# Optimization experiments

Measured on AMD Instinct MI355X. Metric: run time of the kernel, lower is better.

The kernel has to match this reference:

```python
import jax, jax.numpy as jnp
import numpy as np

D_MODEL = 1024
NUM_HEADS = 16
HEAD_DIM = D_MODEL // NUM_HEADS
SEQ_LEN = 2048
THETA = 10000.0


def setup_inputs() -> dict:
    key = jax.random.key(0)
    ks = jax.random.split(key, 9)
    s = 1.0 / np.sqrt(D_MODEL)
    inp = {
        "x": jax.random.normal(ks[0], (2, SEQ_LEN, D_MODEL), dtype=jnp.float32),
        "Wq": jax.random.uniform(ks[1], (D_MODEL, D_MODEL), jnp.float32, -s, s),
        "bq": jax.random.uniform(ks[2], (D_MODEL,), jnp.float32, -s, s),
        "Wk": jax.random.uniform(ks[3], (D_MODEL, D_MODEL), jnp.float32, -s, s),
        "bk": jax.random.uniform(ks[4], (D_MODEL,), jnp.float32, -s, s),
        "Wv": jax.random.uniform(ks[5], (D_MODEL, D_MODEL), jnp.float32, -s, s),
        "bv": jax.random.uniform(ks[6], (D_MODEL,), jnp.float32, -s, s),
        "Wo": jax.random.uniform(ks[7], (D_MODEL, D_MODEL), jnp.float32, -s, s),
        "bo": jax.random.uniform(ks[8], (D_MODEL,), jnp.float32, -s, s),
    }
    return inp


def _rope_cos_sin(seq_len, dim, theta):
    inv_freq = 1.0 / theta ** (jnp.arange(0, dim, 2, dtype=jnp.float32) / dim)  # [dim/2]
    t = jnp.arange(seq_len, dtype=jnp.float32)
    freqs = jnp.outer(t, inv_freq)  # [S, dim/2]
    return jnp.cos(freqs), jnp.sin(freqs)


def _apply_rope(x, cos, sin):
    # x: [B, H, S, head_dim]; interleaved complex pairs (even, odd)
    x2 = x.reshape(*x.shape[:-1], -1, 2)  # [B,H,S,hd/2,2]
    xe, xo = x2[..., 0], x2[..., 1]
    c = cos[None, None, :, :]
    s = sin[None, None, :, :]
    oe = xe * c - xo * s
    oo = xe * s + xo * c
    return jnp.stack([oe, oo], axis=-1).reshape(x.shape)


def reference(x, Wq, bq, Wk, bk, Wv, bv, Wo, bo):
    B, S, D = x.shape
    H, hd = NUM_HEADS, HEAD_DIM
    q = x @ Wq.T + bq
    k = x @ Wk.T + bk
    v = x @ Wv.T + bv
    # [B, H, S, hd]
    q = q.reshape(B, S, H, hd).transpose(0, 2, 1, 3)
    k = k.reshape(B, S, H, hd).transpose(0, 2, 1, 3)
    v = v.reshape(B, S, H, hd).transpose(0, 2, 1, 3)
    cos, sin = _rope_cos_sin(S, hd, THETA)
    q = _apply_rope(q, cos, sin)
    k = _apply_rope(k, cos, sin)
    scores = jnp.einsum("bhqd,bhkd->bhqk", q, k) / jnp.sqrt(jnp.float32(hd))
    causal = jnp.triu(jnp.ones((S, S), dtype=bool), k=1)
    scores = jnp.where(causal[None, None, :, :], -jnp.inf, scores)
    attn = jax.nn.softmax(scores, axis=-1)
    out = jnp.einsum("bhqk,bhkd->bhqd", attn, v)
    out = out.transpose(0, 2, 1, 3).reshape(B, S, D)
    return out @ Wo.T + bo
```

## Files before the change

### kernel.cpp

```cpp
#include <hip/hip_runtime.h>
#include <hip/hip_bf16.h>

#define S_LEN 2048
#define DM 1024
#define NH 16
#define HD 64
#define M_ROWS 4096
#define LOG2E 1.4426950408889634f
#define MASKVAL -1.0e4f
#define QSCALE 0.18033688011112042f

typedef __attribute__((ext_vector_type(8))) short short8;
typedef __attribute__((ext_vector_type(4))) float f32x4;
typedef __attribute__((ext_vector_type(16))) float f32x16;

__device__ inline ushort f2b(float f) {
  union { float f; unsigned u; } v; v.f = f;
  unsigned r = v.u + 0x7fffu + ((v.u >> 16) & 1u);
  return (ushort)(r >> 16);
}

__device__ inline float b2f(ushort u) {
  union { unsigned u; float f; } v; v.u = ((unsigned)u) << 16; return v.f;
}

__device__ inline unsigned pk_bf16(float a, float b) {
  __hip_bfloat162 h = __float22bfloat162_rn(make_float2(a, b));
  union { __hip_bfloat162 h; unsigned u; } v; v.h = h;
  return v.u;
}

__device__ inline float fexp2(float x) { return __builtin_amdgcn_exp2f(x); }

__device__ inline void gl_lds16(const void* g, void* l) {
  __builtin_amdgcn_global_load_lds(
      (const __attribute__((address_space(1))) void*)g,
      (__attribute__((address_space(3))) void*)l, 16, 0, 0);
}

__global__ __launch_bounds__(256) void cast_rope_kernel(
    const float* __restrict__ x, const float* __restrict__ Wq, const float* __restrict__ Wk,
    const float* __restrict__ Wv, const float* __restrict__ Wo,
    ushort* __restrict__ xb, ushort* __restrict__ Wqb, ushort* __restrict__ Wkb,
    ushort* __restrict__ Wvb, ushort* __restrict__ Wob,
    float* __restrict__ ropeC, float* __restrict__ ropeS) {
  const int bid = blockIdx.x;
  if (bid >= 8192) {
    int idx = (bid - 8192) * 256 + threadIdx.x;
    int s = idx >> 5, i = idx & 31;
    float inv = exp2f(-(float)i * (13.287712379549449f / 32.0f));
    float a = (float)s * inv;
    ropeC[idx] = cosf(a);
    ropeS[idx] = sinf(a);
    return;
  }
  int i = bid * 256 + threadIdx.x;
  int r = i >> 18, off = i & 0x3FFFF;
  const float4* s;
  uint2* d;
  switch (r) {
    case 0: case 1: case 2: case 3: s = (const float4*)x + i;  d = (uint2*)xb + i;  break;
    case 4: s = (const float4*)Wq + off; d = (uint2*)Wqb + off; break;
    case 5: s = (const float4*)Wk + off; d = (uint2*)Wkb + off; break;
    case 6: s = (const float4*)Wv + off; d = (uint2*)Wvb + off; break;
    default: s = (const float4*)Wo + off; d = (uint2*)Wob + off; break;
  }
  float4 v = *s;
  uint2 o;
  o.x = pk_bf16(v.x, v.y);
  o.y = pk_bf16(v.z, v.w);
  *d = o;
}

__global__ __launch_bounds__(256) void gemm_qkv_kernel(const ushort* __restrict__ xb,
    const ushort* __restrict__ Wqb, const ushort* __restrict__ Wkb, const ushort* __restrict__ Wvb,
    const float* __restrict__ bq, const float* __restrict__ bk, const float* __restrict__ bv,
    const float* __restrict__ ropeC, const float* __restrict__ ropeS,
    ushort* __restrict__ qb, ushort* __restrict__ kb, ushort* __restrict__ vT) {
  __shared__ ushort lds[128 * 136];
  ushort* As = lds;
  ushort* Bs = lds + 8192;
  const int z = blockIdx.z;
  const ushort* W = (z == 0) ? Wqb : ((z == 1) ? Wkb : Wvb);
  const float* bias = (z == 0) ? bq : ((z == 1) ? bk : bv);
  const int m0 = blockIdx.x * 128, n0 = blockIdx.y * 128;
  const int t = threadIdx.x, lane = t & 63, wave = t >> 6;
  const int wr = (wave >> 1) * 64, wc = (wave & 1) * 64;
  const int lr = lane & 15, lg = lane >> 4;

  int rows_[4], gs_[4], slots_[4];
#pragma unroll
  for (int j = 0; j < 4; j++) {
    const int slot = wave * 256 + j * 64 + lane;
    slots_[j] = slot;
    rows_[j] = slot >> 3;
    gs_[j] = (slot & 7) ^ (rows_[j] & 7);
  }

  f32x4 acc[4][4];
#pragma unroll
  for (int a = 0; a < 4; a++)
#pragma unroll
    for (int b = 0; b < 4; b++) acc[a][b] = (f32x4){0.f, 0.f, 0.f, 0.f};

  for (int k0 = 0; k0 < DM; k0 += 64) {
    __syncthreads();
#pragma unroll
    for (int j = 0; j < 4; j++)
      gl_lds16(&xb[(size_t)(m0 + rows_[j]) * DM + k0 + gs_[j] * 8], &As[slots_[j] * 8]);
#pragma unroll
    for (int j = 0; j < 4; j++)
      gl_lds16(&W[(size_t)(n0 + rows_[j]) * DM + k0 + gs_[j] * 8], &Bs[slots_[j] * 8]);
    __syncthreads();
#pragma unroll
    for (int s32 = 0; s32 < 2; s32++) {
      short8 af[4], bf[4];
#pragma unroll
      for (int mt = 0; mt < 4; mt++) {
        const int row = wr + mt * 16 + lr;
        af[mt] = *(const short8*)&As[(row * 8 + ((s32 * 4 + lg) ^ (row & 7))) * 8];
      }
#pragma unroll
      for (int nt = 0; nt < 4; nt++) {
        const int row = wc + nt * 16 + lr;
        bf[nt] = *(const short8*)&Bs[(row * 8 + ((s32 * 4 + lg) ^ (row & 7))) * 8];
      }
#pragma unroll
      for (int mt = 0; mt < 4; mt++)
#pragma unroll
        for (int nt = 0; nt < 4; nt++)
          acc[mt][nt] = __builtin_amdgcn_mfma_f32_16x16x32_bf16(af[mt], bf[nt], acc[mt][nt], 0, 0, 0);
    }
  }

  __syncthreads();
#pragma unroll
  for (int mt = 0; mt < 4; mt++) {
#pragma unroll
    for (int nt = 0; nt < 4; nt++) {
      const int nloc = wc + nt * 16 + lr;
      const float bn = bias[n0 + nloc];
#pragma unroll
      for (int r = 0; r < 4; r++) {
        const int mloc = wr + mt * 16 + lg * 4 + r;
        const ushort v = f2b(acc[mt][nt][r] + bn);
        if (z < 2) lds[mloc * 136 + nloc] = v;
        else       lds[nloc * 136 + mloc] = v;
      }
    }
  }
  __syncthreads();

  const int b = m0 >> 11;
  if (z < 2) {
    ushort* dst = (z == 0) ? qb : kb;
    const float qscale = (z == 0) ? QSCALE : 1.0f;
#pragma unroll
    for (int c = 0; c < 8; c++) {
      const int sloc = c * 16 + (t >> 4);
      const int nloc = (t & 15) * 8;
      short8 val = *(const short8*)&lds[sloc * 136 + nloc];
      const int s = (m0 + sloc) & (S_LEN - 1);
      const int h = (n0 + nloc) >> 6;
      const int d0 = nloc & 63;
      const float4 cv = *(const float4*)&ropeC[s * 32 + d0 / 2];
      const float4 sv = *(const float4*)&ropeS[s * 32 + d0 / 2];
      uint4 o;
      {
        float e = b2f((ushort)val[0]), od = b2f((ushort)val[1]);
        o.x = pk_bf16((e * cv.x - od * sv.x) * qscale, (e * sv.x + od * cv.x) * qscale);
      }
      {
        float e = b2f((ushort)val[2]), od = b2f((ushort)val[3]);
        o.y = pk_bf16((e * cv.y - od * sv.y) * qscale, (e * sv.y + od * cv.y) * qscale);
      }
      {
        float e = b2f((ushort)val[4]), od = b2f((ushort)val[5]);
        o.z = pk_bf16((e * cv.z - od * sv.z) * qscale, (e * sv.z + od * cv.z) * qscale);
      }
      {
        float e = b2f((ushort)val[6]), od = b2f((ushort)val[7]);
        o.w = pk_bf16((e * cv.w - od * sv.w) * qscale, (e * sv.w + od * cv.w) * qscale);
      }
      *(uint4*)&dst[(((size_t)b * NH + h) * S_LEN + s) * HD + d0] = o;
    }
  } else {
    const int sbase = m0 & (S_LEN - 1);
#pragma unroll
    for (int c = 0; c < 8; c++) {
      const int nloc = c * 16 + (t >> 4);
      const int s0 = (t & 15) * 8;
      short8 val = *(const short8*)&lds[nloc * 136 + s0];
      const int h = (n0 + nloc) >> 6;
      const int d = nloc & 63;
      *(short8*)&vT[(((size_t)b * NH + h) * HD + d) * S_LEN + sbase + s0] = val;
    }
  }
}

__global__ __launch_bounds__(256) void flash_kernel(const ushort* __restrict__ qb,
                                                    const ushort* __restrict__ kb,
                                                    const ushort* __restrict__ vT,
                                                    ushort* __restrict__ Oh,
                                                    float* __restrict__ lsum) {
  __shared__ ushort Ks[2][4096];
  __shared__ ushort VTs[2][4096];
  const int t = threadIdx.x, lane = t & 63, wave = t >> 6;
  const int q31 = lane & 31, h = lane >> 5;
  const int bh = blockIdx.y;
  const int cid = blockIdx.x;
  const int g = (cid >= 24) ? 3 : (cid >= 12) ? 2 : (cid >= 4) ? 1 : 0;
  const int nc = g + 1;
  const int o = cid - 4 * ((g * (g + 1)) >> 1);
  const int qi = o / nc;
  const int c = o - qi * nc;
  const int qt = g * 4 + qi;
  const int q0 = qt * 128;
  const int ntiles = 2 * qt + 2;
  const int kstart = c * 8;
  const int kend = min(kstart + 8, ntiles);
  const int pidx = bh * 40 + cid;

  const ushort* kbh = kb + (size_t)bh * S_LEN * HD;
  const ushort* vbh = vT + (size_t)bh * HD * S_LEN;

  const int qrow = q0 + wave * 32 + q31;
  const ushort* qptr = qb + ((size_t)bh * S_LEN + qrow) * HD + h * 8;
  short8 qf[4];
#pragma unroll
  for (int s = 0; s < 4; s++) qf[s] = *(const short8*)(qptr + s * 16);

  const int slot0 = wave * 128 + lane, slot1 = slot0 + 64;
  const int row0 = slot0 >> 3, g0 = (slot0 & 7) ^ (row0 & 7);
  const int row1 = slot1 >> 3, g1 = (slot1 & 7) ^ (row1 & 7);
  const int lo0 = wave * 128 * 8, lo1 = lo0 + 64 * 8;

  int foff[4][2];
#pragma unroll
  for (int s = 0; s < 4; s++)
#pragma unroll
    for (int st = 0; st < 2; st++) {
      const int row = st * 32 + q31;
      foff[s][st] = (row * 8 + ((2 * s + h) ^ (row & 7))) * 8;
    }

  {
    const int k00 = kstart * 64;
    gl_lds16(kbh + (size_t)(k00 + row0) * HD + g0 * 8, &Ks[0][lo0]);
    gl_lds16(kbh + (size_t)(k00 + row1) * HD + g1 * 8, &Ks[0][lo1]);
    gl_lds16(vbh + (size_t)row0 * S_LEN + k00 + g0 * 8, &VTs[0][lo0]);
    gl_lds16(vbh + (size_t)row1 * S_LEN + k00 + g1 * 8, &VTs[0][lo1]);
  }
  __syncthreads();

  f32x16 O[2];
#pragma unroll
  for (int st = 0; st < 2; st++)
#pragma unroll
    for (int r = 0; r < 16; r++) O[st][r] = 0.f;
  float lacc = 0.f;
  int cur = 0;

  for (int kt = kstart; kt < kend; kt++) {
    if (kt + 1 < kend) {
      const int k0n = (kt + 1) * 64;
      gl_lds16(kbh + (size_t)(k0n + row0) * HD + g0 * 8, &Ks[cur ^ 1][lo0]);
      gl_lds16(kbh + (size_t)(k0n + row1) * HD + g1 * 8, &Ks[cur ^ 1][lo1]);
      gl_lds16(vbh + (size_t)row0 * S_LEN + k0n + g0 * 8, &VTs[cur ^ 1][lo0]);
      gl_lds16(vbh + (size_t)row1 * S_LEN + k0n + g1 * 8, &VTs[cur ^ 1][lo1]);
    }
    const ushort* Kb = Ks[cur];
    const ushort* Vb = VTs[cur];

    f32x16 sc[2];
#pragma unroll
    for (int st = 0; st < 2; st++)
#pragma unroll
      for (int r = 0; r < 16; r++) sc[st][r] = 0.f;
#pragma unroll
    for (int s = 0; s < 4; s++) {
#pragma unroll
      for (int st = 0; st < 2; st++) {
        const short8 kf = *(const short8*)&Kb[foff[s][st]];
        sc[st] = __builtin_amdgcn_mfma_f32_32x32x16_bf16(kf, qf[s], sc[st], 0, 0, 0);
      }
    }
    if (kt * 64 + 63 > q0 + wave * 32) {
#pragma unroll
      for (int st = 0; st < 2; st++)
#pragma unroll
        for (int r = 0; r < 16; r++) {
          const int kcol = kt * 64 + st * 32 + (r & 3) + 8 * (r >> 2) + 4 * h;
          if (kcol > qrow) sc[st][r] = MASKVAL;
        }
    }
#pragma unroll
    for (int st = 0; st < 2; st++)
#pragma unroll
      for (int r = 0; r < 16; r++) {
        const float p = fexp2(sc[st][r]);
        sc[st][r] = p;
        lacc += p;
      }

    unsigned pp[8][2];
#pragma unroll
    for (int st = 0; st < 2; st++)
#pragma unroll
      for (int rg = 0; rg < 4; rg++) {
        pp[st * 4 + rg][0] = pk_bf16(sc[st][4 * rg + 0], sc[st][4 * rg + 1]);
        pp[st * 4 + rg][1] = pk_bf16(sc[st][4 * rg + 2], sc[st][4 * rg + 3]);
      }
#pragma unroll
    for (int s = 0; s < 4; s++) {
      const unsigned sA0 = pp[2 * s][0], sA1 = pp[2 * s][1];
      const unsigned sB0 = pp[2 * s + 1][0], sB1 = pp[2 * s + 1][1];
      const unsigned send0 = h ? sA0 : sB0;
      const unsigned send1 = h ? sA1 : sB1;
      const unsigned recv0 = (unsigned)__shfl_xor((int)send0, 32);
      const unsigned recv1 = (unsigned)__shfl_xor((int)send1, 32);
      union { unsigned u[4]; short8 v; } pf;
      pf.u[0] = h ? recv0 : sA0;
      pf.u[1] = h ? recv1 : sA1;
      pf.u[2] = h ? sB0 : recv0;
      pf.u[3] = h ? sB1 : recv1;
#pragma unroll
      for (int st = 0; st < 2; st++) {
        const short8 vf = *(const short8*)&Vb[foff[s][st]];
        O[st] = __builtin_amdgcn_mfma_f32_32x32x16_bf16(vf, pf.v, O[st], 0, 0, 0);
      }
    }
    __syncthreads();
    cur ^= 1;
  }

  lacc += __shfl_xor(lacc, 32);

  ushort* obase = Oh + ((size_t)pidx * 128 + wave * 32 + q31) * HD;
#pragma unroll
  for (int st = 0; st < 2; st++)
#pragma unroll
    for (int rg = 0; rg < 4; rg++) {
      const int d0 = st * 32 + 8 * rg + 4 * h;
      uint2 w;
      w.x = pk_bf16(O[st][4 * rg + 0], O[st][4 * rg + 1]);
      w.y = pk_bf16(O[st][4 * rg + 2], O[st][4 * rg + 3]);
      *(uint2*)&obase[d0] = w;
    }
  if (h == 0) lsum[(size_t)pidx * 128 + wave * 32 + q31] = lacc;
}

__global__ __launch_bounds__(256) void combine_kernel(const ushort* __restrict__ Oh,
                                                      const float* __restrict__ lsum,
                                                      ushort* __restrict__ attn) {
  const int tid = blockIdx.x * 256 + threadIdx.x;
  const int d8 = tid & 7;
  const int q = (tid >> 3) & (S_LEN - 1);
  const int bh = tid >> 14;
  const int qt = q >> 7, row = q & 127;
  const int g = qt >> 2, nc = g + 1;
  const int base = 4 * ((g * (g + 1)) >> 1) + (qt & 3) * nc;
  const int p0 = bh * 40 + base;

  float l = 0.f;
  float acc[8];
#pragma unroll
  for (int j = 0; j < 8; j++) acc[j] = 0.f;
  for (int c = 0; c < nc; c++) {
    const size_t rowidx = (size_t)(p0 + c) * 128 + row;
    l += lsum[rowidx];
    const uint4 a = *(const uint4*)&Oh[rowidx * HD + d8 * 8];
    const unsigned au[4] = {a.x, a.y, a.z, a.w};
#pragma unroll
    for (int j = 0; j < 4; j++) {
      acc[2 * j] += b2f((ushort)(au[j] & 0xffff));
      acc[2 * j + 1] += b2f((ushort)(au[j] >> 16));
    }
  }
  const float inv = 1.f / l;
  uint4 o;
  unsigned* op = (unsigned*)&o;
#pragma unroll
  for (int j = 0; j < 4; j++) op[j] = pk_bf16(acc[2 * j] * inv, acc[2 * j + 1] * inv);
  const int b = bh >> 4, hh = bh & 15;
  *(uint4*)&attn[((size_t)b * S_LEN + q) * DM + hh * HD + d8 * 8] = o;
}

__global__ __launch_bounds__(256) void gemm_out_kernel(const ushort* __restrict__ attn,
                                                       const ushort* __restrict__ Wob,
                                                       const float* __restrict__ bo,
                                                       float* __restrict__ out) {
  __shared__ ushort As[4096];
  __shared__ ushort Bs[2048];
  const int m0 = blockIdx.x * 128, n0 = blockIdx.y * 64;
  const int t = threadIdx.x, lane = t & 63, wave = t >> 6;
  const int wm = (wave >> 1) * 64, wn = (wave & 1) * 32;
  const int lr = lane & 15, lg = lane >> 4;
  const int slotA0 = wave * 128 + lane, slotA1 = slotA0 + 64;
  const int rowA0 = slotA0 >> 2, gA0 = (slotA0 & 3) ^ (rowA0 & 3);
  const int rowA1 = slotA1 >> 2, gA1 = (slotA1 & 3) ^ (rowA1 & 3);
  const int slotB = wave * 64 + lane;
  const int rowB = slotB >> 2, gB = (slotB & 3) ^ (rowB & 3);

  f32x4 acc[4][2];
#pragma unroll
  for (int a = 0; a < 4; a++)
#pragma unroll
    for (int b = 0; b < 2; b++) acc[a][b] = (f32x4){0.f, 0.f, 0.f, 0.f};

  for (int k0 = 0; k0 < DM; k0 += 32) {
    __syncthreads();
    gl_lds16(&attn[(size_t)(m0 + rowA0) * DM + k0 + gA0 * 8], &As[slotA0 * 8]);
    gl_lds16(&attn[(size_t)(m0 + rowA1) * DM + k0 + gA1 * 8], &As[slotA1 * 8]);
    gl_lds16(&Wob[(size_t)(n0 + rowB) * DM + k0 + gB * 8], &Bs[slotB * 8]);
    __syncthreads();
    short8 af[4], bf[2];
#pragma unroll
    for (int mt = 0; mt < 4; mt++) {
      const int row = wm + mt * 16 + lr;
      af[mt] = *(const short8*)&As[(row * 4 + (lg ^ (row & 3))) * 8];
    }
#pragma unroll
    for (int nt = 0; nt < 2; nt++) {
      const int row = wn + nt * 16 + lr;
      bf[nt] = *(const short8*)&Bs[(row * 4 + (lg ^ (row & 3))) * 8];
    }
#pragma unroll
    for (int mt = 0; mt < 4; mt++)
#pragma unroll
      for (int nt = 0; nt < 2; nt++)
        acc[mt][nt] = __builtin_amdgcn_mfma_f32_16x16x32_bf16(af[mt], bf[nt], acc[mt][nt], 0, 0, 0);
  }

#pragma unroll
  for (int mt = 0; mt < 4; mt++) {
#pragma unroll
    for (int nt = 0; nt < 2; nt++) {
      const int n = n0 + wn + nt * 16 + lr;
      const float bn = bo[n];
#pragma unroll
      for (int r = 0; r < 4; r++) {
        const int m = m0 + wm + mt * 16 + lg * 4 + r;
        out[(size_t)m * DM + n] = acc[mt][nt][r] + bn;
      }
    }
  }
}

extern "C" void kernel_launch(void* const* d_in, const int* in_sizes, int n_in,
                              void* d_out, int out_size, void* d_ws, size_t ws_size,
                              hipStream_t stream) {
  const float* x  = (const float*)d_in[0];
  const float* Wq = (const float*)d_in[1];
  const float* bq = (const float*)d_in[2];
  const float* Wk = (const float*)d_in[3];
  const float* bk = (const float*)d_in[4];
  const float* Wv = (const float*)d_in[5];
  const float* bv = (const float*)d_in[6];
  const float* Wo = (const float*)d_in[7];
  const float* bo = (const float*)d_in[8];
  float* out = (float*)d_out;

  char* ws = (char*)d_ws;
  size_t off = 0;
  auto alloc = [&](size_t bytes) { char* p = ws + off; off += (bytes + 255) & ~255ull; return p; };
  ushort* xb   = (ushort*)alloc((size_t)M_ROWS * DM * 2);
  ushort* Wqb  = (ushort*)alloc((size_t)DM * DM * 2);
  ushort* Wkb  = (ushort*)alloc((size_t)DM * DM * 2);
  ushort* Wvb  = (ushort*)alloc((size_t)DM * DM * 2);
  ushort* Wob  = (ushort*)alloc((size_t)DM * DM * 2);
  ushort* qb   = (ushort*)alloc((size_t)M_ROWS * DM * 2);
  ushort* kb   = (ushort*)alloc((size_t)M_ROWS * DM * 2);
  ushort* vTb  = (ushort*)alloc((size_t)M_ROWS * DM * 2);
  ushort* attn = (ushort*)alloc((size_t)M_ROWS * DM * 2);
  ushort* Ohb  = (ushort*)alloc((size_t)1280 * 128 * HD * 2);
  float* lsb   = (float*)alloc((size_t)1280 * 128 * 4);
  float* ropeC = (float*)alloc((size_t)S_LEN * 32 * 4);
  float* ropeS = (float*)alloc((size_t)S_LEN * 32 * 4);
  (void)ws_size; (void)in_sizes; (void)n_in; (void)out_size;

  cast_rope_kernel<<<8448, 256, 0, stream>>>(x, Wq, Wk, Wv, Wo, xb, Wqb, Wkb, Wvb, Wob,
                                             ropeC, ropeS);
  gemm_qkv_kernel<<<dim3(M_ROWS / 128, DM / 128, 3), 256, 0, stream>>>(
      xb, Wqb, Wkb, Wvb, bq, bk, bv, ropeC, ropeS, qb, kb, vTb);
  flash_kernel<<<dim3(40, 32), 256, 0, stream>>>(qb, kb, vTb, Ohb, lsb);
  combine_kernel<<<2048, 256, 0, stream>>>(Ohb, lsb, attn);
  gemm_out_kernel<<<dim3(M_ROWS / 128, DM / 64), 256, 0, stream>>>(attn, Wob, bo, out);
}
```

Baseline: 202.3 us.

## Double-buffer LDS tiles in QKV and output projection GEMMs

Both projection GEMMs now prefetch the next K-slice into a second LDS buffer while MFMAs run on the current one, so only one barrier is needed per iteration. The QKV GEMM's K-step drops from 64 to 32 so that two buffers fit within the existing 17408-element LDS array, and the swizzle changes to 4 groups per row. The aim is to overlap global-to-LDS loads with compute. The trade-off is twice as many loop iterations and barriers in the QKV kernel, and it relies on the barrier at the end of each iteration to order the async LDS writes.

```diff
diff --git a/kernel.cpp b/kernel.cpp
--- a/kernel.cpp
+++ b/kernel.cpp
@@ -77,7 +77,7 @@
     const float* __restrict__ bq, const float* __restrict__ bk, const float* __restrict__ bv,
     const float* __restrict__ ropeC, const float* __restrict__ ropeS,
     ushort* __restrict__ qb, ushort* __restrict__ kb, ushort* __restrict__ vT) {
-  __shared__ ushort lds[128 * 136];
+  __shared__ ushort lds[17408];
   ushort* As = lds;
   ushort* Bs = lds + 8192;
   const int z = blockIdx.z;
@@ -88,14 +88,13 @@
   const int wr = (wave >> 1) * 64, wc = (wave & 1) * 64;
   const int lr = lane & 15, lg = lane >> 4;
 
-  int rows_[4], gs_[4], slots_[4];
-#pragma unroll
-  for (int j = 0; j < 4; j++) {
-    const int slot = wave * 256 + j * 64 + lane;
-    slots_[j] = slot;
-    rows_[j] = slot >> 3;
-    gs_[j] = (slot & 7) ^ (rows_[j] & 7);
-  }
+  const int slot0 = wave * 128 + lane, slot1 = slot0 + 64;
+  const int row0 = slot0 >> 2, g0 = (slot0 & 3) ^ (row0 & 3);
+  const int row1 = slot1 >> 2, g1 = (slot1 & 3) ^ (row1 & 3);
+  const ushort* Ap0 = &xb[(size_t)(m0 + row0) * DM + g0 * 8];
+  const ushort* Ap1 = &xb[(size_t)(m0 + row1) * DM + g1 * 8];
+  const ushort* Wp0 = &W[(size_t)(n0 + row0) * DM + g0 * 8];
+  const ushort* Wp1 = &W[(size_t)(n0 + row1) * DM + g1 * 8];
 
   f32x4 acc[4][4];
 #pragma unroll
@@ -103,37 +102,43 @@
 #pragma unroll
     for (int b = 0; b < 4; b++) acc[a][b] = (f32x4){0.f, 0.f, 0.f, 0.f};
 
-  for (int k0 = 0; k0 < DM; k0 += 64) {
+  gl_lds16(Ap0, &As[slot0 * 8]);
+  gl_lds16(Ap1, &As[slot1 * 8]);
+  gl_lds16(Wp0, &Bs[slot0 * 8]);
+  gl_lds16(Wp1, &Bs[slot1 * 8]);
+  __syncthreads();
+
+  int buf = 0;
+  for (int i = 0; i < 32; i++) {
+    if (i + 1 < 32) {
+      const int k0 = (i + 1) * 32;
+      const int bo = (buf ^ 1) * 4096;
+      gl_lds16(Ap0 + k0, &As[bo + slot0 * 8]);
+      gl_lds16(Ap1 + k0, &As[bo + slot1 * 8]);
+      gl_lds16(Wp0 + k0, &Bs[bo + slot0 * 8]);
+      gl_lds16(Wp1 + k0, &Bs[bo + slot1 * 8]);
+    }
+    const int fb = buf * 4096;
+    short8 af[4], bf[4];
+#pragma unroll
+    for (int mt = 0; mt < 4; mt++) {
+      const int row = wr + mt * 16 + lr;
+      af[mt] = *(const short8*)&As[fb + (row * 4 + (lg ^ (row & 3))) * 8];
+    }
+#pragma unroll
+    for (int nt = 0; nt < 4; nt++) {
+      const int row = wc + nt * 16 + lr;
+      bf[nt] = *(const short8*)&Bs[fb + (row * 4 + (lg ^ (row & 3))) * 8];
+    }
+#pragma unroll
+    for (int mt = 0; mt < 4; mt++)
+#pragma unroll
+      for (int nt = 0; nt < 4; nt++)
+        acc[mt][nt] = __builtin_amdgcn_mfma_f32_16x16x32_bf16(af[mt], bf[nt], acc[mt][nt], 0, 0, 0);
     __syncthreads();
-#pragma unroll
-    for (int j = 0; j < 4; j++)
-      gl_lds16(&xb[(size_t)(m0 + rows_[j]) * DM + k0 + gs_[j] * 8], &As[slots_[j] * 8]);
-#pragma unroll
-    for (int j = 0; j < 4; j++)
-      gl_lds16(&W[(size_t)(n0 + rows_[j]) * DM + k0 + gs_[j] * 8], &Bs[slots_[j] * 8]);
-    __syncthreads();
-#pragma unroll
-    for (int s32 = 0; s32 < 2; s32++) {
-      short8 af[4], bf[4];
-#pragma unroll
-      for (int mt = 0; mt < 4; mt++) {
-        const int row = wr + mt * 16 + lr;
-        af[mt] = *(const short8*)&As[(row * 8 + ((s32 * 4 + lg) ^ (row & 7))) * 8];
-      }
-#pragma unroll
-      for (int nt = 0; nt < 4; nt++) {
-        const int row = wc + nt * 16 + lr;
-        bf[nt] = *(const short8*)&Bs[(row * 8 + ((s32 * 4 + lg) ^ (row & 7))) * 8];
-      }
-#pragma unroll
-      for (int mt = 0; mt < 4; mt++)
-#pragma unroll
-        for (int nt = 0; nt < 4; nt++)
-          acc[mt][nt] = __builtin_amdgcn_mfma_f32_16x16x32_bf16(af[mt], bf[nt], acc[mt][nt], 0, 0, 0);
-    }
-  }
-
-  __syncthreads();
+    buf ^= 1;
+  }
+
 #pragma unroll
   for (int mt = 0; mt < 4; mt++) {
 #pragma unroll
@@ -390,8 +395,8 @@
                                                        const ushort* __restrict__ Wob,
                                                        const float* __restrict__ bo,
                                                        float* __restrict__ out) {
-  __shared__ ushort As[4096];
-  __shared__ ushort Bs[2048];
+  __shared__ ushort As[2][4096];
+  __shared__ ushort Bs[2][2048];
   const int m0 = blockIdx.x * 128, n0 = blockIdx.y * 64;
   const int t = threadIdx.x, lane = t & 63, wave = t >> 6;
   const int wm = (wave >> 1) * 64, wn = (wave & 1) * 32;
@@ -401,6 +406,9 @@
   const int rowA1 = slotA1 >> 2, gA1 = (slotA1 & 3) ^ (rowA1 & 3);
   const int slotB = wave * 64 + lane;
   const int rowB = slotB >> 2, gB = (slotB & 3) ^ (rowB & 3);
+  const ushort* Ap0 = &attn[(size_t)(m0 + rowA0) * DM + gA0 * 8];
+  const ushort* Ap1 = &attn[(size_t)(m0 + rowA1) * DM + gA1 * 8];
+  const ushort* Wp  = &Wob[(size_t)(n0 + rowB) * DM + gB * 8];
 
   f32x4 acc[4][2];
 #pragma unroll
@@ -408,28 +416,37 @@
 #pragma unroll
     for (int b = 0; b < 2; b++) acc[a][b] = (f32x4){0.f, 0.f, 0.f, 0.f};
 
-  for (int k0 = 0; k0 < DM; k0 += 32) {
-    __syncthreads();
-    gl_lds16(&attn[(size_t)(m0 + rowA0) * DM + k0 + gA0 * 8], &As[slotA0 * 8]);
-    gl_lds16(&attn[(size_t)(m0 + rowA1) * DM + k0 + gA1 * 8], &As[slotA1 * 8]);
-    gl_lds16(&Wob[(size_t)(n0 + rowB) * DM + k0 + gB * 8], &Bs[slotB * 8]);
-    __syncthreads();
+  gl_lds16(Ap0, &As[0][slotA0 * 8]);
+  gl_lds16(Ap1, &As[0][slotA1 * 8]);
+  gl_lds16(Wp, &Bs[0][slotB * 8]);
+  __syncthreads();
+
+  int buf = 0;
+  for (int i = 0; i < 32; i++) {
+    if (i + 1 < 32) {
+      const int k0 = (i + 1) * 32;
+      gl_lds16(Ap0 + k0, &As[buf ^ 1][slotA0 * 8]);
+      gl_lds16(Ap1 + k0, &As[buf ^ 1][slotA1 * 8]);
+      gl_lds16(Wp + k0, &Bs[buf ^ 1][slotB * 8]);
+    }
     short8 af[4], bf[2];
 #pragma unroll
     for (int mt = 0; mt < 4; mt++) {
       const int row = wm + mt * 16 + lr;
-      af[mt] = *(const short8*)&As[(row * 4 + (lg ^ (row & 3))) * 8];
+      af[mt] = *(const short8*)&As[buf][(row * 4 + (lg ^ (row & 3))) * 8];
     }
 #pragma unroll
     for (int nt = 0; nt < 2; nt++) {
       const int row = wn + nt * 16 + lr;
-      bf[nt] = *(const short8*)&Bs[(row * 4 + (lg ^ (row & 3))) * 8];
+      bf[nt] = *(const short8*)&Bs[buf][(row * 4 + (lg ^ (row & 3))) * 8];
     }
 #pragma unroll
     for (int mt = 0; mt < 4; mt++)
 #pragma unroll
       for (int nt = 0; nt < 2; nt++)
         acc[mt][nt] = __builtin_amdgcn_mfma_f32_16x16x32_bf16(af[mt], bf[nt], acc[mt][nt], 0, 0, 0);
+    __syncthreads();
+    buf ^= 1;
   }
 
 #pragma unroll
```

Result: faster. 192.5 us (-4.8%).
